# Performance work log

Measured on AMD Instinct MI355X. Metric: run time of the kernel, lower is better.

## Reference

```python
import jax, jax.numpy as jnp
import numpy as np

NUM_GRAPHS = 64
EPS = 1e-5


def _bn(x, g, b):
    # training-mode BatchNorm1d with biased variance (as torch uses for normalization)
    m = x.mean(axis=0)
    v = x.var(axis=0)
    return (x - m) * jax.lax.rsqrt(v + EPS) * g + b


def setup_inputs() -> dict:
    key = jax.random.key(0)
    ks = jax.random.split(key, 16)
    N, E, F, T, H = 50000, 500000, 8, 8, 64
    d = {
        "x": jax.random.normal(ks[0], (N, F), jnp.float32),
        "edge_index": jax.random.randint(ks[1], (2, E), 0, N),
        "edge_attr": jax.random.uniform(ks[2], (E, T), jnp.float32),
        "batch_index": jnp.sort(jax.random.randint(ks[3], (N,), 0, NUM_GRAPHS)),
        # edge_nn: Linear(T,16) -> ReLU -> Linear(16, F*H)
        "w_e1": jax.random.normal(ks[4], (T, 16), jnp.float32) * 0.2,
        "b_e1": jnp.zeros((16,), jnp.float32),
        "w_e2": jax.random.normal(ks[5], (16, F * H), jnp.float32) * 0.1,
        "b_e2": jnp.zeros((F * H,), jnp.float32),
        # NNConv root weight + bias
        "root": jax.random.normal(ks[6], (F, H), jnp.float32) * 0.2,
        "conv_bias": jnp.zeros((H,), jnp.float32),
        "g_bnc": jnp.ones((H,), jnp.float32), "b_bnc": jnp.zeros((H,), jnp.float32),
        "w1": jax.random.normal(ks[7], (2 * H, 256), jnp.float32) * 0.08,
        "b1": jnp.zeros((256,), jnp.float32),
        "g1": jnp.ones((256,), jnp.float32), "be1": jnp.zeros((256,), jnp.float32),
        "w2": jax.random.normal(ks[8], (256, 128), jnp.float32) * 0.08,
        "b2": jnp.zeros((128,), jnp.float32),
        "g2": jnp.ones((128,), jnp.float32), "be2": jnp.zeros((128,), jnp.float32),
        "w3": jax.random.normal(ks[9], (128, 64), jnp.float32) * 0.1,
        "b3": jnp.zeros((64,), jnp.float32),
        "g3": jnp.ones((64,), jnp.float32), "be3": jnp.zeros((64,), jnp.float32),
        "wout": jax.random.normal(ks[10], (64, 10), jnp.float32) * 0.1,
        "bout": jnp.zeros((10,), jnp.float32),
    }
    return d


def reference(x, edge_index, edge_attr, batch_index,
              w_e1, b_e1, w_e2, b_e2, root, conv_bias, g_bnc, b_bnc,
              w1, b1, g1, be1, w2, b2, g2, be2, w3, b3, g3, be3, wout, bout):
    N, F = x.shape
    H = root.shape[1]
    src, dst = edge_index[0], edge_index[1]

    # edge-conditioned weights: edge_nn(edge_attr) -> [E, F, H]
    h_e = jax.nn.relu(edge_attr @ w_e1 + b_e1)
    W_e = (h_e @ w_e2 + b_e2).reshape(-1, F, H)

    # gather source features, per-edge matmul, scatter-mean into targets
    msg = jnp.einsum('ef,efh->eh', x[src], W_e)            # [E, H]
    agg = jax.ops.segment_sum(msg, dst, num_segments=N)
    deg = jax.ops.segment_sum(jnp.ones((msg.shape[0],), msg.dtype), dst, num_segments=N)
    agg = agg / jnp.maximum(deg, 1.0)[:, None]
    h = x @ root + agg + conv_bias                          # NNConv output [N, H]

    h = jax.nn.relu(_bn(h, g_bnc, b_bnc))

    # global mean + max pooling per graph
    gs = jax.ops.segment_sum(h, batch_index, num_segments=NUM_GRAPHS)
    cnt = jax.ops.segment_sum(jnp.ones((N,), h.dtype), batch_index, num_segments=NUM_GRAPHS)
    gmean = gs / jnp.maximum(cnt, 1.0)[:, None]
    gmax = jax.ops.segment_max(h, batch_index, num_segments=NUM_GRAPHS)
    gmax = jnp.where(cnt[:, None] > 0, gmax, 0.0)
    g = jnp.concatenate([gmean, gmax], axis=1)              # [G, 2H]

    g = jax.nn.relu(_bn(g @ w1 + b1, g1, be1))
    g = jax.nn.relu(_bn(g @ w2 + b2, g2, be2))
    g = jax.nn.relu(_bn(g @ w3 + b3, g3, be3))
    return g @ wout + bout
```

## Files before the change

### kernel.cpp

```cpp
#include <hip/hip_runtime.h>

#define DEG_CAP 64
#define ZROW 144
#define ZPAD 148

__device__ __forceinline__ int rfl(int v) { return __builtin_amdgcn_readfirstlane(v); }

__global__ void k_fill(const int* __restrict__ ei, const float* __restrict__ w_e2,
                       const float* __restrict__ b_e2, const float* __restrict__ root,
                       int* __restrict__ cursor, int2* __restrict__ slots2,
                       float* __restrict__ wlin, int E) {
  int e = blockIdx.x * blockDim.x + threadIdx.x;
  if (e < ZROW * 64) {
    int j = e >> 6, h = e & 63;
    float v;
    if (j < 128) {
      int k = j >> 3, f = (((j >> 1) & 3) << 1) | (j & 1);
      v = w_e2[k * 512 + f * 64 + h];
    } else if (j < 136) {
      v = b_e2[(j - 128) * 64 + h];
    } else {
      v = root[(j - 136) * 64 + h];
    }
    wlin[e] = v;
  }
  if (e >= E) return;
  int dst = ei[E + e];
  int src = ei[e];
  int slot = atomicAdd(&cursor[dst], 1);
  if (slot < DEG_CAP) slots2[(size_t)dst * DEG_CAP + slot] = make_int2(e, src);
}

__global__ void k_zgather(const float* __restrict__ x, const float* __restrict__ ea,
                          const float* __restrict__ w_e1, const float* __restrict__ b_e1,
                          const int* __restrict__ cursor, const int2* __restrict__ slots2,
                          float* __restrict__ zbuf, int N) {
  int lane = threadIdx.x & 63;
  int n = rfl(blockIdx.x * (blockDim.x >> 6) + (threadIdx.x >> 6));
  if (n >= N) return;
  int k = lane >> 2;
  int f2 = (lane & 3) << 1;
  float w1c[8];
#pragma unroll
  for (int t = 0; t < 8; ++t) w1c[t] = w_e1[t * 16 + k];
  float bk = b_e1[k];
  int d = cursor[n];
  int dc = min(d, DEG_CAP);
  int2 sl = (lane < dc) ? slots2[(size_t)n * DEG_CAP + lane] : make_int2(0, 0);
  float z0 = 0.f, z1 = 0.f, xs0 = 0.f, xs1 = 0.f;
  if (dc > 0) {
    int e0 = __shfl(sl.x, 0), s0 = __shfl(sl.y, 0);
    float4 a0 = *reinterpret_cast<const float4*>(ea + (size_t)e0 * 8);
    float4 a1 = *reinterpret_cast<const float4*>(ea + (size_t)e0 * 8 + 4);
    float2 xv = *reinterpret_cast<const float2*>(x + (size_t)s0 * 8 + f2);
    for (int i = 1; i < dc; ++i) {
      int e1 = __shfl(sl.x, i), s1 = __shfl(sl.y, i);
      float4 n0 = *reinterpret_cast<const float4*>(ea + (size_t)e1 * 8);
      float4 n1 = *reinterpret_cast<const float4*>(ea + (size_t)e1 * 8 + 4);
      float2 xn = *reinterpret_cast<const float2*>(x + (size_t)s1 * 8 + f2);
      float he = bk;
      he = fmaf(a0.x, w1c[0], he); he = fmaf(a0.y, w1c[1], he);
      he = fmaf(a0.z, w1c[2], he); he = fmaf(a0.w, w1c[3], he);
      he = fmaf(a1.x, w1c[4], he); he = fmaf(a1.y, w1c[5], he);
      he = fmaf(a1.z, w1c[6], he); he = fmaf(a1.w, w1c[7], he);
      he = fmaxf(he, 0.f);
      z0 = fmaf(he, xv.x, z0); z1 = fmaf(he, xv.y, z1);
      xs0 += xv.x; xs1 += xv.y;
      a0 = n0; a1 = n1; xv = xn;
    }
    float he = bk;
    he = fmaf(a0.x, w1c[0], he); he = fmaf(a0.y, w1c[1], he);
    he = fmaf(a0.z, w1c[2], he); he = fmaf(a0.w, w1c[3], he);
    he = fmaf(a1.x, w1c[4], he); he = fmaf(a1.y, w1c[5], he);
    he = fmaf(a1.z, w1c[6], he); he = fmaf(a1.w, w1c[7], he);
    he = fmaxf(he, 0.f);
    z0 = fmaf(he, xv.x, z0); z1 = fmaf(he, xv.y, z1);
    xs0 += xv.x; xs1 += xv.y;
  }
  float inv = 1.f / (float)max(d, 1);
  z0 *= inv; z1 *= inv; xs0 *= inv; xs1 *= inv;
  float2* zp = reinterpret_cast<float2*>(zbuf + (size_t)n * ZROW);
  zp[lane] = make_float2(z0, z1);
  if (lane < 4) zp[64 + lane] = make_float2(xs0, xs1);
  if (lane < 8) zbuf[(size_t)n * ZROW + 136 + lane] = x[(size_t)n * 8 + lane];
}

__global__ __launch_bounds__(256) void k_zwgemm(
    const float* __restrict__ zbuf, const float* __restrict__ wlin,
    const float* __restrict__ conv_bias, float* __restrict__ hout,
    float* __restrict__ stats, int N) {
  __shared__ float zt[64 * ZPAD];
  __shared__ float sl[128];
  int t = threadIdx.x;
  int n0 = blockIdx.x * 64;

  for (int i4 = t; i4 < 64 * ZROW / 4; i4 += 256) {
    int dw = i4 << 2;
    int r = dw / ZROW;
    int c = dw - r * ZROW;
    float4 v = make_float4(0.f, 0.f, 0.f, 0.f);
    if (n0 + r < N)
      v = *reinterpret_cast<const float4*>(zbuf + (size_t)(n0 + r) * ZROW + c);
    *reinterpret_cast<float4*>(&zt[r * ZPAD + c]) = v;
  }
  if (t < 128) sl[t] = 0.f;
  __syncthreads();

  int hg = t & 15;
  int ng = t >> 4;
  float acc[4][4];
#pragma unroll
  for (int i = 0; i < 4; ++i)
#pragma unroll
    for (int q = 0; q < 4; ++q) acc[i][q] = 0.f;

  for (int j = 0; j < ZROW; j += 4) {
    float4 wv[4];
#pragma unroll
    for (int r = 0; r < 4; ++r)
      wv[r] = *reinterpret_cast<const float4*>(&wlin[(j + r) * 64 + hg * 4]);
    float4 zv[4];
#pragma unroll
    for (int i = 0; i < 4; ++i)
      zv[i] = *reinterpret_cast<const float4*>(&zt[(ng * 4 + i) * ZPAD + j]);
#pragma unroll
    for (int i = 0; i < 4; ++i) {
      acc[i][0] = fmaf(zv[i].x, wv[0].x, acc[i][0]);
      acc[i][1] = fmaf(zv[i].x, wv[0].y, acc[i][1]);
      acc[i][2] = fmaf(zv[i].x, wv[0].z, acc[i][2]);
      acc[i][3] = fmaf(zv[i].x, wv[0].w, acc[i][3]);
      acc[i][0] = fmaf(zv[i].y, wv[1].x, acc[i][0]);
      acc[i][1] = fmaf(zv[i].y, wv[1].y, acc[i][1]);
      acc[i][2] = fmaf(zv[i].y, wv[1].z, acc[i][2]);
      acc[i][3] = fmaf(zv[i].y, wv[1].w, acc[i][3]);
      acc[i][0] = fmaf(zv[i].z, wv[2].x, acc[i][0]);
      acc[i][1] = fmaf(zv[i].z, wv[2].y, acc[i][1]);
      acc[i][2] = fmaf(zv[i].z, wv[2].z, acc[i][2]);
      acc[i][3] = fmaf(zv[i].z, wv[2].w, acc[i][3]);
      acc[i][0] = fmaf(zv[i].w, wv[3].x, acc[i][0]);
      acc[i][1] = fmaf(zv[i].w, wv[3].y, acc[i][1]);
      acc[i][2] = fmaf(zv[i].w, wv[3].z, acc[i][2]);
      acc[i][3] = fmaf(zv[i].w, wv[3].w, acc[i][3]);
    }
  }

  float cb[4];
#pragma unroll
  for (int q = 0; q < 4; ++q) cb[q] = conv_bias[hg * 4 + q];
  float bns[4] = {0.f, 0.f, 0.f, 0.f}, bnq[4] = {0.f, 0.f, 0.f, 0.f};
#pragma unroll
  for (int i = 0; i < 4; ++i) {
    int n = n0 + ng * 4 + i;
    float h0 = acc[i][0] + cb[0], h1 = acc[i][1] + cb[1];
    float h2 = acc[i][2] + cb[2], h3 = acc[i][3] + cb[3];
    if (n < N) {
      *reinterpret_cast<float4*>(&hout[(size_t)n * 64 + hg * 4]) =
          make_float4(h0, h1, h2, h3);
      bns[0] += h0; bns[1] += h1; bns[2] += h2; bns[3] += h3;
      bnq[0] += h0 * h0; bnq[1] += h1 * h1; bnq[2] += h2 * h2; bnq[3] += h3 * h3;
    }
  }
#pragma unroll
  for (int q = 0; q < 4; ++q) {
    bns[q] += __shfl_xor(bns[q], 16); bns[q] += __shfl_xor(bns[q], 32);
    bnq[q] += __shfl_xor(bnq[q], 16); bnq[q] += __shfl_xor(bnq[q], 32);
  }
  if ((t & 48) == 0) {
#pragma unroll
    for (int q = 0; q < 4; ++q) {
      atomicAdd(&sl[hg * 4 + q], bns[q]);
      atomicAdd(&sl[64 + hg * 4 + q], bnq[q]);
    }
  }
  __syncthreads();
  if (t < 128) atomicAdd(&stats[t], sl[t]);
}

__global__ void k_bnpool(const float* __restrict__ hbuf, const float* __restrict__ stats,
                         const int* __restrict__ batch, const float* __restrict__ gamma,
                         const float* __restrict__ beta, float* __restrict__ gsum,
                         unsigned int* __restrict__ gmax, int* __restrict__ gcnt, int N) {
  int lane = threadIdx.x & 63;
  int wid = blockIdx.x * (blockDim.x >> 6) + (threadIdx.x >> 6);
  int nw = gridDim.x * (blockDim.x >> 6);
  float m = stats[lane] / (float)N;
  float var = stats[64 + lane] / (float)N - m * m;
  float rs = rsqrtf(var + 1e-5f);
  float ga = gamma[lane], be = beta[lane];
  int per = (N + nw - 1) / nw;
  int n0 = wid * per;
  int n1 = min(N, n0 + per);
  int cur = -1, cnt = 0;
  float s = 0.f, mx = 0.f;
  for (int n = n0; n < n1; ++n) {
    int g = batch[n];
    float v = hbuf[(size_t)n * 64 + lane];
    float y = fmaxf(fmaf((v - m) * rs, ga, be), 0.f);
    if (g != cur) {
      if (cur >= 0) {
        atomicAdd(&gsum[cur * 64 + lane], s);
        atomicMax(&gmax[cur * 64 + lane], __float_as_uint(mx));
        if (lane == 0) atomicAdd(&gcnt[cur], cnt);
      }
      cur = g; s = 0.f; mx = 0.f; cnt = 0;
    }
    s += y; mx = fmaxf(mx, y); ++cnt;
  }
  if (cur >= 0) {
    atomicAdd(&gsum[cur * 64 + lane], s);
    atomicMax(&gmax[cur * 64 + lane], __float_as_uint(mx));
    if (lane == 0) atomicAdd(&gcnt[cur], cnt);
  }
}

#define PA 132
#define PB 260
__global__ __launch_bounds__(1024) void k_mlphead(
    const float* __restrict__ gsum, const unsigned int* __restrict__ gmaxu,
    const int* __restrict__ gcnt,
    const float* __restrict__ W1, const float* __restrict__ B1,
    const float* __restrict__ G1, const float* __restrict__ E1,
    const float* __restrict__ W2, const float* __restrict__ B2,
    const float* __restrict__ G2, const float* __restrict__ E2,
    const float* __restrict__ W3, const float* __restrict__ B3,
    const float* __restrict__ G3, const float* __restrict__ E3,
    const float* __restrict__ Wo, const float* __restrict__ Bo,
    float* __restrict__ out) {
  __shared__ float A[64 * PA];
  __shared__ float B[64 * PB];
  int t = threadIdx.x;

  for (int i = t; i < 64 * 128; i += 1024) {
    int r = i >> 7, c = i & 127;
    float v;
    if (c < 64) v = gsum[r * 64 + c] / fmaxf((float)gcnt[r], 1.f);
    else v = __uint_as_float(gmaxu[r * 64 + (c - 64)]);
    A[r * PA + c] = v;
  }
  __syncthreads();

  {
    int c = t & 255, rg = t >> 8;
    float acc[16];
    float bb = B1[c];
#pragma unroll
    for (int i = 0; i < 16; ++i) acc[i] = bb;
    for (int k = 0; k < 128; k += 4) {
      float w0 = W1[(k + 0) * 256 + c], w1 = W1[(k + 1) * 256 + c];
      float w2 = W1[(k + 2) * 256 + c], w3 = W1[(k + 3) * 256 + c];
#pragma unroll
      for (int i = 0; i < 16; ++i) {
        float4 gv = *reinterpret_cast<const float4*>(&A[(rg * 16 + i) * PA + k]);
        acc[i] = fmaf(gv.x, w0, acc[i]); acc[i] = fmaf(gv.y, w1, acc[i]);
        acc[i] = fmaf(gv.z, w2, acc[i]); acc[i] = fmaf(gv.w, w3, acc[i]);
      }
    }
#pragma unroll
    for (int i = 0; i < 16; ++i) B[(rg * 16 + i) * PB + c] = acc[i];
  }
  __syncthreads();
  if (t < 256) {
    float s = 0.f, q = 0.f;
    for (int r = 0; r < 64; ++r) { float v = B[r * PB + t]; s += v; q += v * v; }
    float m = s * (1.f / 64.f), var = q * (1.f / 64.f) - m * m;
    float rs = rsqrtf(var + 1e-5f), ga = G1[t], be = E1[t];
    for (int r = 0; r < 64; ++r) {
      float v = B[r * PB + t];
      B[r * PB + t] = fmaxf(fmaf((v - m) * rs, ga, be), 0.f);
    }
  }
  __syncthreads();

  {
    int c = t & 127, rg = t >> 7;
    float acc[8];
    float bb = B2[c];
#pragma unroll
    for (int i = 0; i < 8; ++i) acc[i] = bb;
    for (int k = 0; k < 256; k += 4) {
      float w0 = W2[(k + 0) * 128 + c], w1 = W2[(k + 1) * 128 + c];
      float w2 = W2[(k + 2) * 128 + c], w3 = W2[(k + 3) * 128 + c];
#pragma unroll
      for (int i = 0; i < 8; ++i) {
        float4 v = *reinterpret_cast<const float4*>(&B[(rg * 8 + i) * PB + k]);
        acc[i] = fmaf(v.x, w0, acc[i]); acc[i] = fmaf(v.y, w1, acc[i]);
        acc[i] = fmaf(v.z, w2, acc[i]); acc[i] = fmaf(v.w, w3, acc[i]);
      }
    }
#pragma unroll
    for (int i = 0; i < 8; ++i) A[(rg * 8 + i) * PA + c] = acc[i];
  }
  __syncthreads();
  if (t < 128) {
    float s = 0.f, q = 0.f;
    for (int r = 0; r < 64; ++r) { float v = A[r * PA + t]; s += v; q += v * v; }
    float m = s * (1.f / 64.f), var = q * (1.f / 64.f) - m * m;
    float rs = rsqrtf(var + 1e-5f), ga = G2[t], be = E2[t];
    for (int r = 0; r < 64; ++r) {
      float v = A[r * PA + t];
      A[r * PA + t] = fmaxf(fmaf((v - m) * rs, ga, be), 0.f);
    }
  }
  __syncthreads();

  {
    int c = t & 63, rg = t >> 6;
    float acc[4];
    float bb = B3[c];
#pragma unroll
    for (int i = 0; i < 4; ++i) acc[i] = bb;
    for (int k = 0; k < 128; k += 4) {
      float w0 = W3[(k + 0) * 64 + c], w1 = W3[(k + 1) * 64 + c];
      float w2 = W3[(k + 2) * 64 + c], w3 = W3[(k + 3) * 64 + c];
#pragma unroll
      for (int i = 0; i < 4; ++i) {
        float4 v = *reinterpret_cast<const float4*>(&A[(rg * 4 + i) * PA + k]);
        acc[i] = fmaf(v.x, w0, acc[i]); acc[i] = fmaf(v.y, w1, acc[i]);
        acc[i] = fmaf(v.z, w2, acc[i]); acc[i] = fmaf(v.w, w3, acc[i]);
      }
    }
#pragma unroll
    for (int i = 0; i < 4; ++i) B[(rg * 4 + i) * PB + c] = acc[i];
  }
  __syncthreads();
  if (t < 64) {
    float s = 0.f, q = 0.f;
    for (int r = 0; r < 64; ++r) { float v = B[r * PB + t]; s += v; q += v * v; }
    float m = s * (1.f / 64.f), var = q * (1.f / 64.f) - m * m;
    float rs = rsqrtf(var + 1e-5f), ga = G3[t], be = E3[t];
    for (int r = 0; r < 64; ++r) {
      float v = B[r * PB + t];
      B[r * PB + t] = fmaxf(fmaf((v - m) * rs, ga, be), 0.f);
    }
  }
  __syncthreads();

  if (t < 640) {
    int r = t / 10, c = t - r * 10;
    float a = Bo[c];
#pragma unroll
    for (int k = 0; k < 64; ++k) a = fmaf(B[r * PB + k], Wo[k * 10 + c], a);
    out[r * 10 + c] = a;
  }
}

extern "C" void kernel_launch(void* const* d_in, const int* in_sizes, int n_in,
                              void* d_out, int out_size, void* d_ws, size_t ws_size,
                              hipStream_t stream) {
  const float* x = (const float*)d_in[0];
  const int* ei = (const int*)d_in[1];
  const float* ea = (const float*)d_in[2];
  const int* batch = (const int*)d_in[3];
  const float* w_e1 = (const float*)d_in[4];
  const float* b_e1 = (const float*)d_in[5];
  const float* w_e2 = (const float*)d_in[6];
  const float* b_e2 = (const float*)d_in[7];
  const float* root = (const float*)d_in[8];
  const float* conv_bias = (const float*)d_in[9];
  const float* g_bnc = (const float*)d_in[10];
  const float* b_bnc = (const float*)d_in[11];
  const float* w1 = (const float*)d_in[12];
  const float* b1 = (const float*)d_in[13];
  const float* g1 = (const float*)d_in[14];
  const float* be1 = (const float*)d_in[15];
  const float* w2 = (const float*)d_in[16];
  const float* b2 = (const float*)d_in[17];
  const float* g2 = (const float*)d_in[18];
  const float* be2 = (const float*)d_in[19];
  const float* w3 = (const float*)d_in[20];
  const float* b3 = (const float*)d_in[21];
  const float* g3 = (const float*)d_in[22];
  const float* be3 = (const float*)d_in[23];
  const float* wout = (const float*)d_in[24];
  const float* bout = (const float*)d_in[25];

  int N = in_sizes[0] / 8;
  int E = in_sizes[1] / 2;

  char* wsb = (char*)d_ws;
  size_t off = 0;
  auto alloc = [&](size_t bytes) -> void* {
    void* p = wsb + off;
    off += (bytes + 255) & ~(size_t)255;
    return p;
  };
  size_t zeroBytes = (size_t)N * 4 + 8384 * 4;
  int* cursor = (int*)alloc(zeroBytes);
  float* zblk = (float*)((char*)cursor + (size_t)N * 4);
  float* stats = zblk;
  float* gsum = zblk + 128;
  unsigned int* gmax = (unsigned int*)(zblk + 128 + 4096);
  int* gcnt = (int*)(zblk + 128 + 8192);
  int2* slots2 = (int2*)alloc((size_t)N * DEG_CAP * 8);
  float* wlin = (float*)alloc(ZROW * 64 * 4);
  float* zbuf = (float*)alloc((size_t)N * ZROW * 4);
  float* hbuf = (float*)alloc((size_t)N * 64 * 4);

  hipMemsetAsync(cursor, 0, zeroBytes, stream);

  const int tb = 256;
  k_fill<<<(E + tb - 1) / tb, tb, 0, stream>>>(ei, w_e2, b_e2, root, cursor,
                                               slots2, wlin, E);
  k_zgather<<<(N + 3) / 4, 256, 0, stream>>>(x, ea, w_e1, b_e1, cursor, slots2,
                                             zbuf, N);
  k_zwgemm<<<(N + 63) / 64, 256, 0, stream>>>(zbuf, wlin, conv_bias, hbuf, stats, N);
  k_bnpool<<<512, 256, 0, stream>>>(hbuf, stats, batch, g_bnc, b_bnc, gsum, gmax, gcnt, N);
  k_mlphead<<<1, 1024, 0, stream>>>(gsum, gmax, gcnt,
                                    w1, b1, g1, be1, w2, b2, g2, be2,
                                    w3, b3, g3, be3, wout, bout, (float*)d_out);
}
```

Before: 313.5 us.

## Precompute edge hidden features, stage weights in LDS, split MLP head across blocks

The edge MLP's first layer (ReLU(edge_attr·w_e1+b_e1)) is now computed once per edge in the fill kernel and written to a 16-float buffer. The gather kernel then reads one hidden value per lane instead of recomputing the 8-term dot product for every lane. The node GEMM now stages the weight matrix in shared memory and reads z rows straight from global memory instead of staging z tiles. The single-block 1024-thread MLP head is split into per-layer kernels spread over multiple blocks, with BN statistics reduced inside each block. This trades redundant compute for an extra E×16 float write and read, plus three more kernel launches.

New measurement: 298.4 us. -4.8%, faster.

```diff
diff --git a/kernel.cpp b/kernel.cpp
--- a/kernel.cpp
+++ b/kernel.cpp
@@ -2,14 +2,15 @@
 
 #define DEG_CAP 64
 #define ZROW 144
-#define ZPAD 148
 
 __device__ __forceinline__ int rfl(int v) { return __builtin_amdgcn_readfirstlane(v); }
 
-__global__ void k_fill(const int* __restrict__ ei, const float* __restrict__ w_e2,
-                       const float* __restrict__ b_e2, const float* __restrict__ root,
-                       int* __restrict__ cursor, int2* __restrict__ slots2,
-                       float* __restrict__ wlin, int E) {
+__global__ void k_hefill(const float* __restrict__ ea, const float* __restrict__ w,
+                         const float* __restrict__ b, const int* __restrict__ ei,
+                         const float* __restrict__ w_e2, const float* __restrict__ b_e2,
+                         const float* __restrict__ root, float* __restrict__ he,
+                         int* __restrict__ cursor, int2* __restrict__ slots2,
+                         float* __restrict__ wlin, int E) {
   int e = blockIdx.x * blockDim.x + threadIdx.x;
   if (e < ZROW * 64) {
     int j = e >> 6, h = e & 63;
@@ -29,10 +30,28 @@
   int src = ei[e];
   int slot = atomicAdd(&cursor[dst], 1);
   if (slot < DEG_CAP) slots2[(size_t)dst * DEG_CAP + slot] = make_int2(e, src);
-}
-
-__global__ void k_zgather(const float* __restrict__ x, const float* __restrict__ ea,
-                          const float* __restrict__ w_e1, const float* __restrict__ b_e1,
+  const float4* eap = reinterpret_cast<const float4*>(ea + (size_t)e * 8);
+  float4 a0 = eap[0], a1 = eap[1];
+  float av[8] = {a0.x, a0.y, a0.z, a0.w, a1.x, a1.y, a1.z, a1.w};
+  float o[16];
+#pragma unroll
+  for (int k = 0; k < 16; ++k) o[k] = b[k];
+#pragma unroll
+  for (int t = 0; t < 8; ++t) {
+    float at = av[t];
+#pragma unroll
+    for (int k = 0; k < 16; ++k) o[k] = fmaf(at, w[t * 16 + k], o[k]);
+  }
+#pragma unroll
+  for (int k = 0; k < 16; ++k) o[k] = fmaxf(o[k], 0.f);
+  float4* hp = reinterpret_cast<float4*>(he + (size_t)e * 16);
+  hp[0] = make_float4(o[0], o[1], o[2], o[3]);
+  hp[1] = make_float4(o[4], o[5], o[6], o[7]);
+  hp[2] = make_float4(o[8], o[9], o[10], o[11]);
+  hp[3] = make_float4(o[12], o[13], o[14], o[15]);
+}
+
+__global__ void k_zgather(const float* __restrict__ x, const float* __restrict__ he,
                           const int* __restrict__ cursor, const int2* __restrict__ slots2,
                           float* __restrict__ zbuf, int N) {
   int lane = threadIdx.x & 63;
@@ -40,41 +59,23 @@
   if (n >= N) return;
   int k = lane >> 2;
   int f2 = (lane & 3) << 1;
-  float w1c[8];
-#pragma unroll
-  for (int t = 0; t < 8; ++t) w1c[t] = w_e1[t * 16 + k];
-  float bk = b_e1[k];
   int d = cursor[n];
   int dc = min(d, DEG_CAP);
   int2 sl = (lane < dc) ? slots2[(size_t)n * DEG_CAP + lane] : make_int2(0, 0);
   float z0 = 0.f, z1 = 0.f, xs0 = 0.f, xs1 = 0.f;
   if (dc > 0) {
     int e0 = __shfl(sl.x, 0), s0 = __shfl(sl.y, 0);
-    float4 a0 = *reinterpret_cast<const float4*>(ea + (size_t)e0 * 8);
-    float4 a1 = *reinterpret_cast<const float4*>(ea + (size_t)e0 * 8 + 4);
+    float hk = he[(size_t)e0 * 16 + k];
     float2 xv = *reinterpret_cast<const float2*>(x + (size_t)s0 * 8 + f2);
     for (int i = 1; i < dc; ++i) {
       int e1 = __shfl(sl.x, i), s1 = __shfl(sl.y, i);
-      float4 n0 = *reinterpret_cast<const float4*>(ea + (size_t)e1 * 8);
-      float4 n1 = *reinterpret_cast<const float4*>(ea + (size_t)e1 * 8 + 4);
-      float2 xn = *reinterpret_cast<const float2*>(x + (size_t)s1 * 8 + f2);
-      float he = bk;
-      he = fmaf(a0.x, w1c[0], he); he = fmaf(a0.y, w1c[1], he);
-      he = fmaf(a0.z, w1c[2], he); he = fmaf(a0.w, w1c[3], he);
-      he = fmaf(a1.x, w1c[4], he); he = fmaf(a1.y, w1c[5], he);
-      he = fmaf(a1.z, w1c[6], he); he = fmaf(a1.w, w1c[7], he);
-      he = fmaxf(he, 0.f);
-      z0 = fmaf(he, xv.x, z0); z1 = fmaf(he, xv.y, z1);
+      float hk2 = he[(size_t)e1 * 16 + k];
+      float2 xv2 = *reinterpret_cast<const float2*>(x + (size_t)s1 * 8 + f2);
+      z0 = fmaf(hk, xv.x, z0); z1 = fmaf(hk, xv.y, z1);
       xs0 += xv.x; xs1 += xv.y;
-      a0 = n0; a1 = n1; xv = xn;
-    }
-    float he = bk;
-    he = fmaf(a0.x, w1c[0], he); he = fmaf(a0.y, w1c[1], he);
-    he = fmaf(a0.z, w1c[2], he); he = fmaf(a0.w, w1c[3], he);
-    he = fmaf(a1.x, w1c[4], he); he = fmaf(a1.y, w1c[5], he);
-    he = fmaf(a1.z, w1c[6], he); he = fmaf(a1.w, w1c[7], he);
-    he = fmaxf(he, 0.f);
-    z0 = fmaf(he, xv.x, z0); z1 = fmaf(he, xv.y, z1);
+      hk = hk2; xv = xv2;
+    }
+    z0 = fmaf(hk, xv.x, z0); z1 = fmaf(hk, xv.y, z1);
     xs0 += xv.x; xs1 += xv.y;
   }
   float inv = 1.f / (float)max(d, 1);
@@ -89,20 +90,14 @@
     const float* __restrict__ zbuf, const float* __restrict__ wlin,
     const float* __restrict__ conv_bias, float* __restrict__ hout,
     float* __restrict__ stats, int N) {
-  __shared__ float zt[64 * ZPAD];
+  __shared__ float wt[ZROW * 64];
   __shared__ float sl[128];
   int t = threadIdx.x;
   int n0 = blockIdx.x * 64;
 
-  for (int i4 = t; i4 < 64 * ZROW / 4; i4 += 256) {
-    int dw = i4 << 2;
-    int r = dw / ZROW;
-    int c = dw - r * ZROW;
-    float4 v = make_float4(0.f, 0.f, 0.f, 0.f);
-    if (n0 + r < N)
-      v = *reinterpret_cast<const float4*>(zbuf + (size_t)(n0 + r) * ZROW + c);
-    *reinterpret_cast<float4*>(&zt[r * ZPAD + c]) = v;
-  }
+  for (int i4 = t; i4 < ZROW * 16; i4 += 256)
+    *reinterpret_cast<float4*>(&wt[i4 << 2]) =
+        *reinterpret_cast<const float4*>(&wlin[i4 << 2]);
   if (t < 128) sl[t] = 0.f;
   __syncthreads();
 
@@ -114,15 +109,21 @@
 #pragma unroll
     for (int q = 0; q < 4; ++q) acc[i][q] = 0.f;
 
+  const float* zb0 = zbuf + (size_t)(n0 + ng * 4) * ZROW;
+  bool full = (n0 + 63 < N);
   for (int j = 0; j < ZROW; j += 4) {
     float4 wv[4];
 #pragma unroll
     for (int r = 0; r < 4; ++r)
-      wv[r] = *reinterpret_cast<const float4*>(&wlin[(j + r) * 64 + hg * 4]);
+      wv[r] = *reinterpret_cast<const float4*>(&wt[(j + r) * 64 + hg * 4]);
     float4 zv[4];
 #pragma unroll
-    for (int i = 0; i < 4; ++i)
-      zv[i] = *reinterpret_cast<const float4*>(&zt[(ng * 4 + i) * ZPAD + j]);
+    for (int i = 0; i < 4; ++i) {
+      if (full || n0 + ng * 4 + i < N)
+        zv[i] = *reinterpret_cast<const float4*>(zb0 + (size_t)i * ZROW + j);
+      else
+        zv[i] = make_float4(0.f, 0.f, 0.f, 0.f);
+    }
 #pragma unroll
     for (int i = 0; i < 4; ++i) {
       acc[i][0] = fmaf(zv[i].x, wv[0].x, acc[i][0]);
@@ -213,135 +214,173 @@
   }
 }
 
-#define PA 132
-#define PB 260
-__global__ __launch_bounds__(1024) void k_mlphead(
+__global__ __launch_bounds__(256) void k_head1(
     const float* __restrict__ gsum, const unsigned int* __restrict__ gmaxu,
-    const int* __restrict__ gcnt,
-    const float* __restrict__ W1, const float* __restrict__ B1,
-    const float* __restrict__ G1, const float* __restrict__ E1,
-    const float* __restrict__ W2, const float* __restrict__ B2,
-    const float* __restrict__ G2, const float* __restrict__ E2,
-    const float* __restrict__ W3, const float* __restrict__ B3,
-    const float* __restrict__ G3, const float* __restrict__ E3,
-    const float* __restrict__ Wo, const float* __restrict__ Bo,
-    float* __restrict__ out) {
-  __shared__ float A[64 * PA];
-  __shared__ float B[64 * PB];
+    const int* __restrict__ gcnt, const float* __restrict__ W1,
+    const float* __restrict__ B1, const float* __restrict__ G1,
+    const float* __restrict__ E1, float* __restrict__ l1) {
+  __shared__ float gb[64 * 132];
+  __shared__ float ws[128 * 16];
+  __shared__ float red[2 * 256];
+  __shared__ float sc[16], sh[16];
   int t = threadIdx.x;
-
-  for (int i = t; i < 64 * 128; i += 1024) {
+  int c0 = blockIdx.x * 16;
+  for (int i = t; i < 64 * 128; i += 256) {
     int r = i >> 7, c = i & 127;
-    float v;
-    if (c < 64) v = gsum[r * 64 + c] / fmaxf((float)gcnt[r], 1.f);
-    else v = __uint_as_float(gmaxu[r * 64 + (c - 64)]);
-    A[r * PA + c] = v;
-  }
-  __syncthreads();
-
-  {
-    int c = t & 255, rg = t >> 8;
-    float acc[16];
-    float bb = B1[c];
-#pragma unroll
-    for (int i = 0; i < 16; ++i) acc[i] = bb;
-    for (int k = 0; k < 128; k += 4) {
-      float w0 = W1[(k + 0) * 256 + c], w1 = W1[(k + 1) * 256 + c];
-      float w2 = W1[(k + 2) * 256 + c], w3 = W1[(k + 3) * 256 + c];
-#pragma unroll
-      for (int i = 0; i < 16; ++i) {
-        float4 gv = *reinterpret_cast<const float4*>(&A[(rg * 16 + i) * PA + k]);
-        acc[i] = fmaf(gv.x, w0, acc[i]); acc[i] = fmaf(gv.y, w1, acc[i]);
-        acc[i] = fmaf(gv.z, w2, acc[i]); acc[i] = fmaf(gv.w, w3, acc[i]);
-      }
-    }
-#pragma unroll
-    for (int i = 0; i < 16; ++i) B[(rg * 16 + i) * PB + c] = acc[i];
-  }
-  __syncthreads();
-  if (t < 256) {
-    float s = 0.f, q = 0.f;
-    for (int r = 0; r < 64; ++r) { float v = B[r * PB + t]; s += v; q += v * v; }
-    float m = s * (1.f / 64.f), var = q * (1.f / 64.f) - m * m;
-    float rs = rsqrtf(var + 1e-5f), ga = G1[t], be = E1[t];
-    for (int r = 0; r < 64; ++r) {
-      float v = B[r * PB + t];
-      B[r * PB + t] = fmaxf(fmaf((v - m) * rs, ga, be), 0.f);
-    }
-  }
-  __syncthreads();
-
-  {
-    int c = t & 127, rg = t >> 7;
-    float acc[8];
-    float bb = B2[c];
-#pragma unroll
-    for (int i = 0; i < 8; ++i) acc[i] = bb;
-    for (int k = 0; k < 256; k += 4) {
-      float w0 = W2[(k + 0) * 128 + c], w1 = W2[(k + 1) * 128 + c];
-      float w2 = W2[(k + 2) * 128 + c], w3 = W2[(k + 3) * 128 + c];
-#pragma unroll
-      for (int i = 0; i < 8; ++i) {
-        float4 v = *reinterpret_cast<const float4*>(&B[(rg * 8 + i) * PB + k]);
-        acc[i] = fmaf(v.x, w0, acc[i]); acc[i] = fmaf(v.y, w1, acc[i]);
-        acc[i] = fmaf(v.z, w2, acc[i]); acc[i] = fmaf(v.w, w3, acc[i]);
-      }
-    }
-#pragma unroll
-    for (int i = 0; i < 8; ++i) A[(rg * 8 + i) * PA + c] = acc[i];
-  }
-  __syncthreads();
-  if (t < 128) {
-    float s = 0.f, q = 0.f;
-    for (int r = 0; r < 64; ++r) { float v = A[r * PA + t]; s += v; q += v * v; }
-    float m = s * (1.f / 64.f), var = q * (1.f / 64.f) - m * m;
-    float rs = rsqrtf(var + 1e-5f), ga = G2[t], be = E2[t];
-    for (int r = 0; r < 64; ++r) {
-      float v = A[r * PA + t];
-      A[r * PA + t] = fmaxf(fmaf((v - m) * rs, ga, be), 0.f);
-    }
-  }
-  __syncthreads();
-
-  {
-    int c = t & 63, rg = t >> 6;
-    float acc[4];
-    float bb = B3[c];
-#pragma unroll
-    for (int i = 0; i < 4; ++i) acc[i] = bb;
-    for (int k = 0; k < 128; k += 4) {
-      float w0 = W3[(k + 0) * 64 + c], w1 = W3[(k + 1) * 64 + c];
-      float w2 = W3[(k + 2) * 64 + c], w3 = W3[(k + 3) * 64 + c];
-#pragma unroll
-      for (int i = 0; i < 4; ++i) {
-        float4 v = *reinterpret_cast<const float4*>(&A[(rg * 4 + i) * PA + k]);
-        acc[i] = fmaf(v.x, w0, acc[i]); acc[i] = fmaf(v.y, w1, acc[i]);
-        acc[i] = fmaf(v.z, w2, acc[i]); acc[i] = fmaf(v.w, w3, acc[i]);
-      }
-    }
-#pragma unroll
-    for (int i = 0; i < 4; ++i) B[(rg * 4 + i) * PB + c] = acc[i];
-  }
-  __syncthreads();
-  if (t < 64) {
-    float s = 0.f, q = 0.f;
-    for (int r = 0; r < 64; ++r) { float v = B[r * PB + t]; s += v; q += v * v; }
-    float m = s * (1.f / 64.f), var = q * (1.f / 64.f) - m * m;
-    float rs = rsqrtf(var + 1e-5f), ga = G3[t], be = E3[t];
-    for (int r = 0; r < 64; ++r) {
-      float v = B[r * PB + t];
-      B[r * PB + t] = fmaxf(fmaf((v - m) * rs, ga, be), 0.f);
-    }
-  }
-  __syncthreads();
-
-  if (t < 640) {
-    int r = t / 10, c = t - r * 10;
-    float a = Bo[c];
-#pragma unroll
-    for (int k = 0; k < 64; ++k) a = fmaf(B[r * PB + k], Wo[k * 10 + c], a);
-    out[r * 10 + c] = a;
-  }
+    float v = (c < 64) ? gsum[r * 64 + c] / fmaxf((float)gcnt[r], 1.f)
+                       : __uint_as_float(gmaxu[r * 64 + (c - 64)]);
+    gb[r * 132 + c] = v;
+  }
+  for (int i = t; i < 128 * 16; i += 256) {
+    int k = i >> 4, ci = i & 15;
+    ws[i] = W1[k * 256 + c0 + ci];
+  }
+  __syncthreads();
+  int ci = t & 15, rg = t >> 4;
+  float acc[4];
+  float bb = B1[c0 + ci];
+#pragma unroll
+  for (int i = 0; i < 4; ++i) acc[i] = bb;
+  for (int kk = 0; kk < 128; kk += 4) {
+    float w0 = ws[kk * 16 + ci], w1 = ws[(kk + 1) * 16 + ci];
+    float w2 = ws[(kk + 2) * 16 + ci], w3 = ws[(kk + 3) * 16 + ci];
+#pragma unroll
+    for (int i = 0; i < 4; ++i) {
+      float4 g4 = *reinterpret_cast<const float4*>(&gb[(rg + 16 * i) * 132 + kk]);
+      acc[i] = fmaf(g4.x, w0, acc[i]); acc[i] = fmaf(g4.y, w1, acc[i]);
+      acc[i] = fmaf(g4.z, w2, acc[i]); acc[i] = fmaf(g4.w, w3, acc[i]);
+    }
+  }
+  float s = 0.f, q = 0.f;
+#pragma unroll
+  for (int i = 0; i < 4; ++i) { s += acc[i]; q += acc[i] * acc[i]; }
+  red[t] = s; red[256 + t] = q;
+  __syncthreads();
+  if (t < 16) {
+    float S = 0.f, Q = 0.f;
+    for (int r = 0; r < 16; ++r) { S += red[r * 16 + t]; Q += red[256 + r * 16 + t]; }
+    float m = S * (1.f / 64.f), v = Q * (1.f / 64.f) - m * m;
+    float rs = rsqrtf(v + 1e-5f);
+    float scale = G1[c0 + t] * rs;
+    sc[t] = scale; sh[t] = E1[c0 + t] - m * scale;
+  }
+  __syncthreads();
+#pragma unroll
+  for (int i = 0; i < 4; ++i)
+    l1[(rg + 16 * i) * 256 + c0 + ci] = fmaxf(fmaf(acc[i], sc[ci], sh[ci]), 0.f);
+}
+
+__global__ __launch_bounds__(256) void k_head2(
+    const float* __restrict__ l1, const float* __restrict__ W2,
+    const float* __restrict__ B2, const float* __restrict__ G2,
+    const float* __restrict__ E2, float* __restrict__ l2) {
+  __shared__ float ab[64 * 260];
+  __shared__ float ws[256 * 8];
+  __shared__ float red[2 * 256];
+  __shared__ float sc[8], sh[8];
+  int t = threadIdx.x;
+  int c0 = blockIdx.x * 8;
+  for (int i4 = t; i4 < 64 * 64; i4 += 256) {
+    int r = i4 >> 6, c4 = (i4 & 63) << 2;
+    *reinterpret_cast<float4*>(&ab[r * 260 + c4]) =
+        *reinterpret_cast<const float4*>(&l1[r * 256 + c4]);
+  }
+  for (int i = t; i < 256 * 8; i += 256) {
+    int k = i >> 3, ci = i & 7;
+    ws[i] = W2[k * 128 + c0 + ci];
+  }
+  __syncthreads();
+  int ci = t & 7, rg = t >> 3;
+  float acc[2];
+  float bb = B2[c0 + ci];
+  acc[0] = bb; acc[1] = bb;
+  for (int kk = 0; kk < 256; kk += 4) {
+    float w0 = ws[kk * 8 + ci], w1 = ws[(kk + 1) * 8 + ci];
+    float w2 = ws[(kk + 2) * 8 + ci], w3 = ws[(kk + 3) * 8 + ci];
+#pragma unroll
+    for (int i = 0; i < 2; ++i) {
+      float4 a4 = *reinterpret_cast<const float4*>(&ab[(rg + 32 * i) * 260 + kk]);
+      acc[i] = fmaf(a4.x, w0, acc[i]); acc[i] = fmaf(a4.y, w1, acc[i]);
+      acc[i] = fmaf(a4.z, w2, acc[i]); acc[i] = fmaf(a4.w, w3, acc[i]);
+    }
+  }
+  float s = acc[0] + acc[1], q = acc[0] * acc[0] + acc[1] * acc[1];
+  red[t] = s; red[256 + t] = q;
+  __syncthreads();
+  if (t < 8) {
+    float S = 0.f, Q = 0.f;
+    for (int r = 0; r < 32; ++r) { S += red[r * 8 + t]; Q += red[256 + r * 8 + t]; }
+    float m = S * (1.f / 64.f), v = Q * (1.f / 64.f) - m * m;
+    float rs = rsqrtf(v + 1e-5f);
+    float scale = G2[c0 + t] * rs;
+    sc[t] = scale; sh[t] = E2[c0 + t] - m * scale;
+  }
+  __syncthreads();
+#pragma unroll
+  for (int i = 0; i < 2; ++i)
+    l2[(rg + 32 * i) * 128 + c0 + ci] = fmaxf(fmaf(acc[i], sc[ci], sh[ci]), 0.f);
+}
+
+__global__ __launch_bounds__(256) void k_head3(
+    const float* __restrict__ l2, const float* __restrict__ W3,
+    const float* __restrict__ B3, const float* __restrict__ G3,
+    const float* __restrict__ E3, float* __restrict__ l3) {
+  __shared__ float ab[64 * 132];
+  __shared__ float ws[128 * 8];
+  __shared__ float red[2 * 256];
+  __shared__ float sc[8], sh[8];
+  int t = threadIdx.x;
+  int c0 = blockIdx.x * 8;
+  for (int i4 = t; i4 < 64 * 32; i4 += 256) {
+    int r = i4 >> 5, c4 = (i4 & 31) << 2;
+    *reinterpret_cast<float4*>(&ab[r * 132 + c4]) =
+        *reinterpret_cast<const float4*>(&l2[r * 128 + c4]);
+  }
+  for (int i = t; i < 128 * 8; i += 256) {
+    int k = i >> 3, ci = i & 7;
+    ws[i] = W3[k * 64 + c0 + ci];
+  }
+  __syncthreads();
+  int ci = t & 7, rg = t >> 3;
+  float acc[2];
+  float bb = B3[c0 + ci];
+  acc[0] = bb; acc[1] = bb;
+  for (int kk = 0; kk < 128; kk += 4) {
+    float w0 = ws[kk * 8 + ci], w1 = ws[(kk + 1) * 8 + ci];
+    float w2 = ws[(kk + 2) * 8 + ci], w3 = ws[(kk + 3) * 8 + ci];
+#pragma unroll
+    for (int i = 0; i < 2; ++i) {
+      float4 a4 = *reinterpret_cast<const float4*>(&ab[(rg + 32 * i) * 132 + kk]);
+      acc[i] = fmaf(a4.x, w0, acc[i]); acc[i] = fmaf(a4.y, w1, acc[i]);
+      acc[i] = fmaf(a4.z, w2, acc[i]); acc[i] = fmaf(a4.w, w3, acc[i]);
+    }
+  }
+  float s = acc[0] + acc[1], q = acc[0] * acc[0] + acc[1] * acc[1];
+  red[t] = s; red[256 + t] = q;
+  __syncthreads();
+  if (t < 8) {
+    float S = 0.f, Q = 0.f;
+    for (int r = 0; r < 32; ++r) { S += red[r * 8 + t]; Q += red[256 + r * 8 + t]; }
+    float m = S * (1.f / 64.f), v = Q * (1.f / 64.f) - m * m;
+    float rs = rsqrtf(v + 1e-5f);
+    float scale = G3[c0 + t] * rs;
+    sc[t] = scale; sh[t] = E3[c0 + t] - m * scale;
+  }
+  __syncthreads();
+#pragma unroll
+  for (int i = 0; i < 2; ++i)
+    l3[(rg + 32 * i) * 64 + c0 + ci] = fmaxf(fmaf(acc[i], sc[ci], sh[ci]), 0.f);
+}
+
+__global__ void k_out(const float* __restrict__ in, const float* __restrict__ W,
+                      const float* __restrict__ b, float* __restrict__ out) {
+  int t = threadIdx.x;
+  if (t >= 640) return;
+  int r = t / 10, c = t % 10;
+  float a = b[c];
+#pragma unroll
+  for (int k = 0; k < 64; ++k) a = fmaf(in[r * 64 + k], W[k * 10 + c], a);
+  out[t] = a;
 }
 
 extern "C" void kernel_launch(void* const* d_in, const int* in_sizes, int n_in,
@@ -391,21 +430,25 @@
   float* gsum = zblk + 128;
   unsigned int* gmax = (unsigned int*)(zblk + 128 + 4096);
   int* gcnt = (int*)(zblk + 128 + 8192);
+  float* he = (float*)alloc((size_t)E * 16 * 4);
   int2* slots2 = (int2*)alloc((size_t)N * DEG_CAP * 8);
   float* wlin = (float*)alloc(ZROW * 64 * 4);
   float* zbuf = (float*)alloc((size_t)N * ZROW * 4);
   float* hbuf = (float*)alloc((size_t)N * 64 * 4);
+  float* l1 = (float*)alloc(64 * 256 * 4);
+  float* l2 = (float*)alloc(64 * 128 * 4);
+  float* l3 = (float*)alloc(64 * 64 * 4);
 
   hipMemsetAsync(cursor, 0, zeroBytes, stream);
 
   const int tb = 256;
-  k_fill<<<(E + tb - 1) / tb, tb, 0, stream>>>(ei, w_e2, b_e2, root, cursor,
-                                               slots2, wlin, E);
-  k_zgather<<<(N + 3) / 4, 256, 0, stream>>>(x, ea, w_e1, b_e1, cursor, slots2,
-                                             zbuf, N);
+  k_hefill<<<(E + tb - 1) / tb, tb, 0, stream>>>(ea, w_e1, b_e1, ei, w_e2, b_e2,
+                                                 root, he, cursor, slots2, wlin, E);
+  k_zgather<<<(N + 3) / 4, 256, 0, stream>>>(x, he, cursor, slots2, zbuf, N);
   k_zwgemm<<<(N + 63) / 64, 256, 0, stream>>>(zbuf, wlin, conv_bias, hbuf, stats, N);
   k_bnpool<<<512, 256, 0, stream>>>(hbuf, stats, batch, g_bnc, b_bnc, gsum, gmax, gcnt, N);
-  k_mlphead<<<1, 1024, 0, stream>>>(gsum, gmax, gcnt,
-                                    w1, b1, g1, be1, w2, b2, g2, be2,
-                                    w3, b3, g3, be3, wout, bout, (float*)d_out);
-}
+  k_head1<<<16, 256, 0, stream>>>(gsum, gmax, gcnt, w1, b1, g1, be1, l1);
+  k_head2<<<16, 256, 0, stream>>>(l1, w2, b2, g2, be2, l2);
+  k_head3<<<8, 256, 0, stream>>>(l2, w3, b3, g3, be3, l3);
+  k_out<<<1, 640, 0, stream>>>(l3, wout, bout, (float*)d_out);
+}
```
